# Kernel optimization log

Hardware: AMD Instinct MI355X
Metric: run time of the kernel (lower is better)

The kernel has to match this reference:

```python
import jax, jax.numpy as jnp
import numpy as np

BN_EPS = 1e-5


def _gin_layer(x, agg, W1, b1, W2, b2, gamma, beta):
    # GINConv with eps=0: h = MLP(x + sum_{j in N(i)} x_j)
    h = x + agg
    h = jax.nn.relu(h @ W1 + b1)
    h = jax.nn.relu(h @ W2 + b2)
    # BatchNorm1d, training mode (batch statistics, biased variance)
    mean = jnp.mean(h, axis=0)
    var = jnp.var(h, axis=0)
    return (h - mean) * jax.lax.rsqrt(var + BN_EPS) * gamma + beta


def setup_inputs() -> dict:
    key = jax.random.key(0)
    ks = jax.random.split(key, 10)
    N, E, D_IN, D_H, D_OUT = 100000, 1600000, 128, 128, 128
    s = lambda fi, fo: (2.0 / (fi + fo)) ** 0.5
    return {
        "x": jax.random.normal(ks[0], (N, D_IN), dtype=jnp.float32),
        "edge_index": jax.random.randint(ks[1], (2, E), 0, N, dtype=jnp.int64),
        "W1a": jax.random.normal(ks[2], (D_IN, D_H), dtype=jnp.float32) * s(D_IN, D_H),
        "b1a": jnp.zeros((D_H,), jnp.float32),
        "W1b": jax.random.normal(ks[3], (D_H, D_H), dtype=jnp.float32) * s(D_H, D_H),
        "b1b": jnp.zeros((D_H,), jnp.float32),
        "g1": jnp.ones((D_H,), jnp.float32),
        "be1": jnp.zeros((D_H,), jnp.float32),
        "W2a": jax.random.normal(ks[4], (D_H, D_H), dtype=jnp.float32) * s(D_H, D_H),
        "b2a": jnp.zeros((D_H,), jnp.float32),
        "W2b": jax.random.normal(ks[5], (D_H, D_OUT), dtype=jnp.float32) * s(D_H, D_OUT),
        "b2b": jnp.zeros((D_OUT,), jnp.float32),
        "g2": jnp.ones((D_OUT,), jnp.float32),
        "be2": jnp.zeros((D_OUT,), jnp.float32),
    }


def reference(x, edge_index, W1a, b1a, W1b, b1b, g1, be1,
              W2a, b2a, W2b, b2b, g2, be2):
    N = x.shape[0]
    src, dst = edge_index[0], edge_index[1]
    # layer 1: scatter-add neighbor features into targets
    agg = jax.ops.segment_sum(x[src], dst, num_segments=N)
    h = _gin_layer(x, agg, W1a, b1a, W1b, b1b, g1, be1)
    # layer 2
    agg = jax.ops.segment_sum(h[src], dst, num_segments=N)
    h = _gin_layer(h, agg, W2a, b2a, W2b, b2b, g2, be2)
    return h
```

## Files before the change

### kernel.cpp

```cpp
#include <hip/hip_runtime.h>
#include <hip/hip_bf16.h>

typedef unsigned int u32;
typedef unsigned short u16;
typedef short bf16x8 __attribute__((ext_vector_type(8)));
typedef float f32x4 __attribute__((ext_vector_type(4)));

static __device__ __forceinline__ float bf_lo(u32 v) { return __uint_as_float(v << 16); }
static __device__ __forceinline__ float bf_hi(u32 v) { return __uint_as_float(v & 0xffff0000u); }
static __device__ __forceinline__ u16 f2bf(float f) {
    u32 u = __float_as_uint(f);
    u32 r = u + 0x7fffu + ((u >> 16) & 1u);
    return (u16)(r >> 16);
}
static __device__ __forceinline__ u32 pack2(float a, float b) {
    return ((u32)f2bf(b) << 16) | (u32)f2bf(a);
}

__global__ __launch_bounds__(256) void convert_k(const float* __restrict__ in,
                                                 u32* __restrict__ out2, int total4)
{
    for (int i = blockIdx.x * 256 + threadIdx.x; i < total4; i += gridDim.x * 256) {
        float4 v = reinterpret_cast<const float4*>(in)[i];
        out2[2 * i + 0] = pack2(v.x, v.y);
        out2[2 * i + 1] = pack2(v.z, v.w);
    }
}

__global__ __launch_bounds__(256) void wprep_k(const float* __restrict__ Wa,
                                               const float* __restrict__ Wb,
                                               const float* __restrict__ Wc,
                                               const float* __restrict__ Wd,
                                               u16* __restrict__ Wf)
{
    int g = blockIdx.x * 256 + threadIdx.x;
    int which = g >> 14;
    int t = g & 16383;
    const float* W = which == 0 ? Wa : which == 1 ? Wb : which == 2 ? Wc : Wd;
    int j  = t & 7;
    int l  = (t >> 3) & 63;
    int nb = (t >> 9) & 7;
    int kg = (t >> 12) & 3;
    int k  = kg * 32 + (l >> 4) * 8 + j;
    int n  = nb * 16 + (l & 15);
    Wf[g] = f2bf(W[k * 128 + n]);
}

__global__ __launch_bounds__(256) void bhist_k(const int* __restrict__ edst,
                                               int* __restrict__ gcount, int E, int NB)
{
    __shared__ int lh[1024];
    for (int i = threadIdx.x; i < 1024; i += 256) lh[i] = 0;
    __syncthreads();
    for (int e = blockIdx.x * 256 + threadIdx.x; e < E; e += gridDim.x * 256)
        atomicAdd(&lh[edst[e] >> 7], 1);
    __syncthreads();
    for (int b = threadIdx.x; b < NB; b += 256)
        if (lh[b]) atomicAdd(&gcount[b], lh[b]);
}

__global__ __launch_bounds__(1024) void bscan_k(const int* __restrict__ gcount,
                                                int* __restrict__ goffs,
                                                int* __restrict__ gcur, int NB)
{
    __shared__ int s[1024];
    int t = threadIdx.x;
    int v = (t < NB) ? gcount[t] : 0;
    s[t] = v; __syncthreads();
    for (int d = 1; d < 1024; d <<= 1) {
        int x = (t >= d) ? s[t - d] : 0;
        __syncthreads();
        s[t] += x;
        __syncthreads();
    }
    if (t < NB) { int o = s[t] - v; goffs[t] = o; gcur[t] = o; }
    if (t == NB - 1) goffs[NB] = s[t];
}

__global__ __launch_bounds__(256) void bfill_k(const int* __restrict__ esrc,
                                               const int* __restrict__ edst,
                                               int* __restrict__ gcur,
                                               u32* __restrict__ bpacked, int E, int NB)
{
    __shared__ int lh[1024];
    __shared__ int lbase[1024];
    int t = threadIdx.x;
    for (int i = t; i < 1024; i += 256) lh[i] = 0;
    __syncthreads();
    int per = (E + gridDim.x - 1) / gridDim.x;
    int lo = blockIdx.x * per;
    int hi = lo + per; if (hi > E) hi = E;
    for (int e = lo + t; e < hi; e += 256) atomicAdd(&lh[edst[e] >> 7], 1);
    __syncthreads();
    for (int b = t; b < NB; b += 256) {
        int c = lh[b];
        lbase[b] = c ? atomicAdd(&gcur[b], c) : 0;
    }
    __syncthreads();
    for (int i = t; i < 1024; i += 256) lh[i] = 0;
    __syncthreads();
    for (int e = lo + t; e < hi; e += 256) {
        int d = edst[e];
        int b = d >> 7;
        int idx = atomicAdd(&lh[b], 1);
        bpacked[lbase[b] + idx] = ((u32)(d & 127) << 17) | (u32)esrc[e];
    }
}

__global__ __launch_bounds__(256) void fsort_k(const u32* __restrict__ bpacked,
                                               const int* __restrict__ goffs,
                                               int* __restrict__ slots,
                                               int* __restrict__ offs,
                                               int* __restrict__ deg, int N)
{
    __shared__ int cnt[128];
    __shared__ int roff[128];
    int b = blockIdx.x, t = threadIdx.x;
    int start = goffs[b], end = goffs[b + 1];
    if (t < 128) cnt[t] = 0;
    __syncthreads();
    for (int e = start + t; e < end; e += 256)
        atomicAdd(&cnt[bpacked[e] >> 17], 1);
    __syncthreads();
    if (t == 0) {
        int acc = 0;
        for (int i = 0; i < 128; ++i) { roff[i] = acc; acc += cnt[i]; }
    }
    __syncthreads();
    int row0 = b * 128;
    if (t < 128 && row0 + t < N) {
        offs[row0 + t] = start + roff[t];
        deg[row0 + t]  = cnt[t];
    }
    if (t < 128) cnt[t] = 0;
    __syncthreads();
    for (int e = start + t; e < end; e += 256) {
        u32 pk = bpacked[e];
        int local = (int)(pk >> 17);
        int idx = atomicAdd(&cnt[local], 1);
        slots[start + roff[local] + idx] = (int)(pk & 0x1FFFF);
    }
}

template<int MODE>
__global__ __launch_bounds__(256) void gather_k(const u32* __restrict__ xb2,
                                                const int* __restrict__ offs,
                                                const int* __restrict__ deg,
                                                const int* __restrict__ slots,
                                                const float* __restrict__ stats_in,
                                                const float* __restrict__ g_in,
                                                const float* __restrict__ be_in,
                                                u32* __restrict__ xa2, int N)
{
    __shared__ float sc[128], sh[128];
    int t = threadIdx.x;
    if (MODE == 1) {
        if (t < 128) {
            float invN = 1.0f / (float)N;
            float mean = stats_in[t] * invN;
            float var  = stats_in[128 + t] * invN - mean * mean;
            float s = g_in[t] * rsqrtf(var + 1e-5f);
            sc[t] = s;
            sh[t] = be_in[t] - mean * s;
        }
        __syncthreads();
    }

    int row = blockIdx.x * 4 + (t >> 6);
    if (row >= N) return;
    int lane = t & 63;

    u32 self = xb2[(size_t)row * 64 + lane];
    float ax0 = bf_lo(self), ay0 = bf_hi(self);
    float ax1 = 0.f, ay1 = 0.f;

    int start = offs[row];
    int dg = deg[row];
    for (int base = 0; base < dg; base += 64) {
        int rem = dg - base;
        int m = rem < 64 ? rem : 64;
        int slot = (lane < m) ? slots[start + base + lane] : 0;
        int j = 0;
        for (; j + 8 <= m; j += 8) {
            int s0 = __shfl(slot, j + 0);
            int s1 = __shfl(slot, j + 1);
            int s2 = __shfl(slot, j + 2);
            int s3 = __shfl(slot, j + 3);
            int s4 = __shfl(slot, j + 4);
            int s5 = __shfl(slot, j + 5);
            int s6 = __shfl(slot, j + 6);
            int s7 = __shfl(slot, j + 7);
            u32 v0 = xb2[(size_t)s0 * 64 + lane];
            u32 v1 = xb2[(size_t)s1 * 64 + lane];
            u32 v2 = xb2[(size_t)s2 * 64 + lane];
            u32 v3 = xb2[(size_t)s3 * 64 + lane];
            u32 v4 = xb2[(size_t)s4 * 64 + lane];
            u32 v5 = xb2[(size_t)s5 * 64 + lane];
            u32 v6 = xb2[(size_t)s6 * 64 + lane];
            u32 v7 = xb2[(size_t)s7 * 64 + lane];
            ax0 += bf_lo(v0); ay0 += bf_hi(v0);
            ax1 += bf_lo(v1); ay1 += bf_hi(v1);
            ax0 += bf_lo(v2); ay0 += bf_hi(v2);
            ax1 += bf_lo(v3); ay1 += bf_hi(v3);
            ax0 += bf_lo(v4); ay0 += bf_hi(v4);
            ax1 += bf_lo(v5); ay1 += bf_hi(v5);
            ax0 += bf_lo(v6); ay0 += bf_hi(v6);
            ax1 += bf_lo(v7); ay1 += bf_hi(v7);
        }
        for (; j < m; ++j) {
            int s = __shfl(slot, j);
            u32 v = xb2[(size_t)s * 64 + lane];
            ax0 += bf_lo(v);
            ay0 += bf_hi(v);
        }
    }
    float ax = ax0 + ax1, ay = ay0 + ay1;
    if (MODE == 1) {
        float d1 = (float)(dg + 1);
        ax = sc[2 * lane]     * ax + d1 * sh[2 * lane];
        ay = sc[2 * lane + 1] * ay + d1 * sh[2 * lane + 1];
    }
    xa2[(size_t)row * 64 + lane] = pack2(ax, ay);
}

template<int MODE>
__global__ __launch_bounds__(256) void mlp_mfma_k(
    const u16* __restrict__ xa,
    const u16* __restrict__ wfa, const float* __restrict__ ba,
    const u16* __restrict__ wfb, const float* __restrict__ bb,
    u16* __restrict__ hb_out, float* __restrict__ hf_out,
    float* __restrict__ partial, int N)
{
    __shared__ short ta[64 * 128];
    __shared__ float ssum[256];

    int t = threadIdx.x;
    int w = t >> 6, l = t & 63;
    int row0 = blockIdx.x * 64;

    for (int c = t; c < 1024; c += 256) {
        int r = c >> 4, ci = c & 15;
        int dst = (r * 128 + ci * 8) ^ ((r & 7) << 3);
        f32x4 v;
        if (row0 + r < N)
            v = *reinterpret_cast<const f32x4*>(xa + ((size_t)(row0 + r) * 128 + ci * 8));
        else
            v = f32x4{0.f, 0.f, 0.f, 0.f};
        *reinterpret_cast<f32x4*>(ta + dst) = v;
    }

    bf16x8 wf[2][4];
#pragma unroll
    for (int nr = 0; nr < 2; ++nr) {
        int nb = 2 * w + nr;
#pragma unroll
        for (int kg = 0; kg < 4; ++kg)
            wf[nr][kg] = *reinterpret_cast<const bf16x8*>(
                wfa + ((size_t)((kg * 8 + nb) * 64 + l)) * 8);
    }
    __syncthreads();

    int rr = l & 15;
    int kg8 = l >> 4;

    f32x4 acc[4][2];
#pragma unroll
    for (int mr = 0; mr < 4; ++mr)
#pragma unroll
        for (int nr = 0; nr < 2; ++nr)
            acc[mr][nr] = f32x4{0.f, 0.f, 0.f, 0.f};

#pragma unroll
    for (int mr = 0; mr < 4; ++mr) {
        int r = mr * 16 + rr;
        bf16x8 af[4];
#pragma unroll
        for (int kg = 0; kg < 4; ++kg) {
            int idx = (r * 128 + kg * 32 + kg8 * 8) ^ ((r & 7) << 3);
            af[kg] = *reinterpret_cast<const bf16x8*>(ta + idx);
        }
#pragma unroll
        for (int nr = 0; nr < 2; ++nr)
#pragma unroll
            for (int kg = 0; kg < 4; ++kg)
                acc[mr][nr] = __builtin_amdgcn_mfma_f32_16x16x32_bf16(
                    af[kg], wf[nr][kg], acc[mr][nr], 0, 0, 0);
    }
    __syncthreads();

    int colb = w * 32;
    float b0 = ba[colb + rr];
    float b1 = ba[colb + 16 + rr];
#pragma unroll
    for (int mr = 0; mr < 4; ++mr)
#pragma unroll
        for (int nr = 0; nr < 2; ++nr) {
            float bb_ = nr ? b1 : b0;
            int col = colb + nr * 16 + rr;
#pragma unroll
            for (int reg = 0; reg < 4; ++reg) {
                int row = mr * 16 + kg8 * 4 + reg;
                float v = fmaxf(acc[mr][nr][reg] + bb_, 0.0f);
                ta[(row * 128 + col) ^ ((row & 7) << 3)] = (short)f2bf(v);
            }
        }

#pragma unroll
    for (int nr = 0; nr < 2; ++nr) {
        int nb = 2 * w + nr;
#pragma unroll
        for (int kg = 0; kg < 4; ++kg)
            wf[nr][kg] = *reinterpret_cast<const bf16x8*>(
                wfb + ((size_t)((kg * 8 + nb) * 64 + l)) * 8);
    }
    __syncthreads();

#pragma unroll
    for (int mr = 0; mr < 4; ++mr)
#pragma unroll
        for (int nr = 0; nr < 2; ++nr)
            acc[mr][nr] = f32x4{0.f, 0.f, 0.f, 0.f};

#pragma unroll
    for (int mr = 0; mr < 4; ++mr) {
        int r = mr * 16 + rr;
        bf16x8 af[4];
#pragma unroll
        for (int kg = 0; kg < 4; ++kg) {
            int idx = (r * 128 + kg * 32 + kg8 * 8) ^ ((r & 7) << 3);
            af[kg] = *reinterpret_cast<const bf16x8*>(ta + idx);
        }
#pragma unroll
        for (int nr = 0; nr < 2; ++nr)
#pragma unroll
            for (int kg = 0; kg < 4; ++kg)
                acc[mr][nr] = __builtin_amdgcn_mfma_f32_16x16x32_bf16(
                    af[kg], wf[nr][kg], acc[mr][nr], 0, 0, 0);
    }

    float c0 = bb[colb + rr];
    float c1 = bb[colb + 16 + rr];
    float s0 = 0.f, q0 = 0.f, s1 = 0.f, q1 = 0.f;
#pragma unroll
    for (int mr = 0; mr < 4; ++mr) {
#pragma unroll
        for (int reg = 0; reg < 4; ++reg) {
            int row = row0 + mr * 16 + kg8 * 4 + reg;
            bool ok = row < N;
            float v0 = fmaxf(acc[mr][0][reg] + c0, 0.0f);
            float v1 = fmaxf(acc[mr][1][reg] + c1, 0.0f);
            if (ok) {
                if (MODE == 0) {
                    hb_out[(size_t)row * 128 + colb + rr]      = f2bf(v0);
                    hb_out[(size_t)row * 128 + colb + 16 + rr] = f2bf(v1);
                } else {
                    hf_out[(size_t)row * 128 + colb + rr]      = v0;
                    hf_out[(size_t)row * 128 + colb + 16 + rr] = v1;
                }
                s0 += v0; q0 += v0 * v0;
                s1 += v1; q1 += v1 * v1;
            }
        }
    }
    s0 += __shfl_xor(s0, 16); s0 += __shfl_xor(s0, 32);
    q0 += __shfl_xor(q0, 16); q0 += __shfl_xor(q0, 32);
    s1 += __shfl_xor(s1, 16); s1 += __shfl_xor(s1, 32);
    q1 += __shfl_xor(q1, 16); q1 += __shfl_xor(q1, 32);
    if (kg8 == 0) {
        ssum[colb + rr]            = s0;
        ssum[128 + colb + rr]      = q0;
        ssum[colb + 16 + rr]       = s1;
        ssum[128 + colb + 16 + rr] = q1;
    }
    __syncthreads();
    partial[(size_t)blockIdx.x * 256 + t] = ssum[t];
}

__global__ __launch_bounds__(256) void reduce_k(const float* __restrict__ partial,
                                                float* __restrict__ stats, int nrows)
{
    int t = threadIdx.x;
    int chunk = (nrows + gridDim.x - 1) / gridDim.x;
    int lo = blockIdx.x * chunk;
    int hi = lo + chunk; if (hi > nrows) hi = nrows;
    float acc = 0.f;
    for (int r = lo; r < hi; ++r)
        acc += partial[(size_t)r * 256 + t];
    if (hi > lo) atomicAdd(&stats[t], acc);
}

__global__ __launch_bounds__(256) void bn_apply_k(
    float* __restrict__ h, const float* __restrict__ stats,
    const float* __restrict__ gamma, const float* __restrict__ beta, int N)
{
    __shared__ float sc[128], sh[128];
    int t = threadIdx.x;
    if (t < 128) {
        float invN = 1.0f / (float)N;
        float mean = stats[t] * invN;
        float var  = stats[128 + t] * invN - mean * mean;
        float s = gamma[t] * rsqrtf(var + 1e-5f);
        sc[t] = s;
        sh[t] = beta[t] - mean * s;
    }
    __syncthreads();
    int total = N * 32;
    for (int i = blockIdx.x * 256 + t; i < total; i += gridDim.x * 256) {
        float4 v = reinterpret_cast<float4*>(h)[i];
        int c = (i & 31) * 4;
        v.x = v.x * sc[c + 0] + sh[c + 0];
        v.y = v.y * sc[c + 1] + sh[c + 1];
        v.z = v.z * sc[c + 2] + sh[c + 2];
        v.w = v.w * sc[c + 3] + sh[c + 3];
        reinterpret_cast<float4*>(h)[i] = v;
    }
}

extern "C" void kernel_launch(void* const* d_in, const int* in_sizes, int n_in,
                              void* d_out, int out_size, void* d_ws, size_t ws_size,
                              hipStream_t stream)
{
    const float* x   = (const float*)d_in[0];
    const int*   ei  = (const int*)d_in[1];
    const float* W1a = (const float*)d_in[2];
    const float* b1a = (const float*)d_in[3];
    const float* W1b = (const float*)d_in[4];
    const float* b1b = (const float*)d_in[5];
    const float* g1  = (const float*)d_in[6];
    const float* be1 = (const float*)d_in[7];
    const float* W2a = (const float*)d_in[8];
    const float* b2a = (const float*)d_in[9];
    const float* W2b = (const float*)d_in[10];
    const float* b2b = (const float*)d_in[11];
    const float* g2  = (const float*)d_in[12];
    const float* be2 = (const float*)d_in[13];

    const int N = in_sizes[0] / 128;
    const int E = in_sizes[1] / 2;
    const int* esrc = ei;
    const int* edst = ei + E;
    const int NB = (N + 127) >> 7;

    const int mblocks = (N + 63) / 64;
    const int gblocks = (N + 3) / 4;

    char* p = (char*)d_ws;
    const size_t featb = (size_t)N * 128 * sizeof(u16);
    u16* xa = (u16*)p;            p += featb;
    u16* h1 = (u16*)p;            p += featb;
    u16* xb = (u16*)p;            p += featb;
    u16* wf = (u16*)p;            p += 4 * 16384 * sizeof(u16);
    int* slots = (int*)p;         p += (size_t)E * sizeof(int);
    int* deg   = (int*)p;         p += (size_t)N * sizeof(int);
    int* offs  = (int*)p;         p += (size_t)N * sizeof(int);
    int* gcount = (int*)p;        p += 1024 * sizeof(int);
    int* goffs  = (int*)p;        p += 1032 * sizeof(int);
    int* gcur   = (int*)p;        p += 1024 * sizeof(int);
    float* stats = (float*)p;     p += 512 * sizeof(float);
    float* partial = (float*)p;   p += (size_t)mblocks * 256 * sizeof(float);
    u32* bpacked = (u32*)xa;

    u16* wf1a = wf;
    u16* wf1b = wf + 16384;
    u16* wf2a = wf + 32768;
    u16* wf2b = wf + 49152;
    float* stats1 = stats;
    float* stats2 = stats + 256;

    float* h = (float*)d_out;

    hipMemsetAsync(gcount, 0, 1024 * sizeof(int), stream);
    bhist_k<<<256, 256, 0, stream>>>(edst, gcount, E, NB);
    bscan_k<<<1, 1024, 0, stream>>>(gcount, goffs, gcur, NB);
    bfill_k<<<256, 256, 0, stream>>>(esrc, edst, gcur, bpacked, E, NB);
    fsort_k<<<NB, 256, 0, stream>>>(bpacked, goffs, slots, offs, deg, N);
    convert_k<<<2048, 256, 0, stream>>>(x, (u32*)xb, N * 32);
    wprep_k<<<256, 256, 0, stream>>>(W1a, W1b, W2a, W2b, wf);
    hipMemsetAsync(stats, 0, 512 * sizeof(float), stream);

    gather_k<0><<<gblocks, 256, 0, stream>>>((const u32*)xb, offs, deg, slots,
                                             nullptr, nullptr, nullptr, (u32*)xa, N);
    mlp_mfma_k<0><<<mblocks, 256, 0, stream>>>(xa, wf1a, b1a, wf1b, b1b,
                                               h1, (float*)nullptr, partial, N);
    reduce_k<<<32, 256, 0, stream>>>(partial, stats1, mblocks);

    gather_k<1><<<gblocks, 256, 0, stream>>>((const u32*)h1, offs, deg, slots,
                                             stats1, g1, be1, (u32*)xa, N);
    mlp_mfma_k<1><<<mblocks, 256, 0, stream>>>(xa, wf2a, b2a, wf2b, b2b,
                                               (u16*)nullptr, h, partial, N);
    reduce_k<<<32, 256, 0, stream>>>(partial, stats2, mblocks);

    bn_apply_k<<<2048, 256, 0, stream>>>(h, stats2, g2, be2, N);
}
```

Before: 299.2 us.

## Use scalar slot loads in gather, bf16 layer-2 output, parallel scan in fsort

The gather kernel now makes the row's offset and degree wave-uniform and loads neighbor indices as scalar loads instead of shuffling them. It unrolls the neighbor loop 16 wide with four accumulator pairs and uses byte-shift addressing for rows. The second MLP now writes bf16 into the h1 buffer instead of fp32 to the output, and a new BN-apply kernel reads bf16 and writes fp32, cutting the intermediate write traffic. fsort's serial per-block prefix sum becomes a parallel Hillis-Steele scan. Storing the pre-BN layer-2 activations in bf16 adds rounding error to the final output.

```diff
diff --git a/kernel.cpp b/kernel.cpp
--- a/kernel.cpp
+++ b/kernel.cpp
@@ -115,6 +115,7 @@
 {
     __shared__ int cnt[128];
     __shared__ int roff[128];
+    __shared__ int sb[128];
     int b = blockIdx.x, t = threadIdx.x;
     int start = goffs[b], end = goffs[b + 1];
     if (t < 128) cnt[t] = 0;
@@ -122,10 +123,15 @@
     for (int e = start + t; e < end; e += 256)
         atomicAdd(&cnt[bpacked[e] >> 17], 1);
     __syncthreads();
-    if (t == 0) {
-        int acc = 0;
-        for (int i = 0; i < 128; ++i) { roff[i] = acc; acc += cnt[i]; }
-    }
+    if (t < 128) sb[t] = cnt[t];
+    __syncthreads();
+    for (int d = 1; d < 128; d <<= 1) {
+        int x = (t < 128 && t >= d) ? sb[t - d] : 0;
+        __syncthreads();
+        if (t < 128) sb[t] += x;
+        __syncthreads();
+    }
+    if (t < 128) roff[t] = sb[t] - cnt[t];
     __syncthreads();
     int row0 = b * 128;
     if (t < 128 && row0 + t < N) {
@@ -141,6 +147,8 @@
         slots[start + roff[local] + idx] = (int)(pk & 0x1FFFF);
     }
 }
+
+#define ROWP(s) reinterpret_cast<const u32*>(xbase + ((size_t)(u32)(s) << 8))
 
 template<int MODE>
 __global__ __launch_bounds__(256) void gather_k(const u32* __restrict__ xb2,
@@ -169,67 +177,87 @@
     int row = blockIdx.x * 4 + (t >> 6);
     if (row >= N) return;
     int lane = t & 63;
-
-    u32 self = xb2[(size_t)row * 64 + lane];
+    const char* xbase = (const char*)xb2;
+
+    u32 self = ROWP(row)[lane];
     float ax0 = bf_lo(self), ay0 = bf_hi(self);
-    float ax1 = 0.f, ay1 = 0.f;
-
-    int start = offs[row];
-    int dg = deg[row];
-    for (int base = 0; base < dg; base += 64) {
-        int rem = dg - base;
-        int m = rem < 64 ? rem : 64;
-        int slot = (lane < m) ? slots[start + base + lane] : 0;
-        int j = 0;
-        for (; j + 8 <= m; j += 8) {
-            int s0 = __shfl(slot, j + 0);
-            int s1 = __shfl(slot, j + 1);
-            int s2 = __shfl(slot, j + 2);
-            int s3 = __shfl(slot, j + 3);
-            int s4 = __shfl(slot, j + 4);
-            int s5 = __shfl(slot, j + 5);
-            int s6 = __shfl(slot, j + 6);
-            int s7 = __shfl(slot, j + 7);
-            u32 v0 = xb2[(size_t)s0 * 64 + lane];
-            u32 v1 = xb2[(size_t)s1 * 64 + lane];
-            u32 v2 = xb2[(size_t)s2 * 64 + lane];
-            u32 v3 = xb2[(size_t)s3 * 64 + lane];
-            u32 v4 = xb2[(size_t)s4 * 64 + lane];
-            u32 v5 = xb2[(size_t)s5 * 64 + lane];
-            u32 v6 = xb2[(size_t)s6 * 64 + lane];
-            u32 v7 = xb2[(size_t)s7 * 64 + lane];
-            ax0 += bf_lo(v0); ay0 += bf_hi(v0);
-            ax1 += bf_lo(v1); ay1 += bf_hi(v1);
-            ax0 += bf_lo(v2); ay0 += bf_hi(v2);
-            ax1 += bf_lo(v3); ay1 += bf_hi(v3);
-            ax0 += bf_lo(v4); ay0 += bf_hi(v4);
-            ax1 += bf_lo(v5); ay1 += bf_hi(v5);
-            ax0 += bf_lo(v6); ay0 += bf_hi(v6);
-            ax1 += bf_lo(v7); ay1 += bf_hi(v7);
-        }
-        for (; j < m; ++j) {
-            int s = __shfl(slot, j);
-            u32 v = xb2[(size_t)s * 64 + lane];
-            ax0 += bf_lo(v);
-            ay0 += bf_hi(v);
-        }
-    }
-    float ax = ax0 + ax1, ay = ay0 + ay1;
+    float ax1 = 0.f, ay1 = 0.f, ax2 = 0.f, ay2 = 0.f, ax3 = 0.f, ay3 = 0.f;
+
+    int ustart = __builtin_amdgcn_readfirstlane(offs[row]);
+    int udg    = __builtin_amdgcn_readfirstlane(deg[row]);
+
+    int e = 0;
+    for (; e + 16 <= udg; e += 16) {
+        int s0 = slots[ustart + e + 0],  s1 = slots[ustart + e + 1];
+        int s2 = slots[ustart + e + 2],  s3 = slots[ustart + e + 3];
+        int s4 = slots[ustart + e + 4],  s5 = slots[ustart + e + 5];
+        int s6 = slots[ustart + e + 6],  s7 = slots[ustart + e + 7];
+        int s8 = slots[ustart + e + 8],  s9 = slots[ustart + e + 9];
+        int sA = slots[ustart + e + 10], sB = slots[ustart + e + 11];
+        int sC = slots[ustart + e + 12], sD = slots[ustart + e + 13];
+        int sE = slots[ustart + e + 14], sF = slots[ustart + e + 15];
+        u32 v0 = ROWP(s0)[lane], v1 = ROWP(s1)[lane];
+        u32 v2 = ROWP(s2)[lane], v3 = ROWP(s3)[lane];
+        u32 v4 = ROWP(s4)[lane], v5 = ROWP(s5)[lane];
+        u32 v6 = ROWP(s6)[lane], v7 = ROWP(s7)[lane];
+        u32 v8 = ROWP(s8)[lane], v9 = ROWP(s9)[lane];
+        u32 vA = ROWP(sA)[lane], vB = ROWP(sB)[lane];
+        u32 vC = ROWP(sC)[lane], vD = ROWP(sD)[lane];
+        u32 vE = ROWP(sE)[lane], vF = ROWP(sF)[lane];
+        ax0 += bf_lo(v0); ay0 += bf_hi(v0);  ax1 += bf_lo(v1); ay1 += bf_hi(v1);
+        ax2 += bf_lo(v2); ay2 += bf_hi(v2);  ax3 += bf_lo(v3); ay3 += bf_hi(v3);
+        ax0 += bf_lo(v4); ay0 += bf_hi(v4);  ax1 += bf_lo(v5); ay1 += bf_hi(v5);
+        ax2 += bf_lo(v6); ay2 += bf_hi(v6);  ax3 += bf_lo(v7); ay3 += bf_hi(v7);
+        ax0 += bf_lo(v8); ay0 += bf_hi(v8);  ax1 += bf_lo(v9); ay1 += bf_hi(v9);
+        ax2 += bf_lo(vA); ay2 += bf_hi(vA);  ax3 += bf_lo(vB); ay3 += bf_hi(vB);
+        ax0 += bf_lo(vC); ay0 += bf_hi(vC);  ax1 += bf_lo(vD); ay1 += bf_hi(vD);
+        ax2 += bf_lo(vE); ay2 += bf_hi(vE);  ax3 += bf_lo(vF); ay3 += bf_hi(vF);
+    }
+    if (e + 8 <= udg) {
+        int s0 = slots[ustart + e + 0], s1 = slots[ustart + e + 1];
+        int s2 = slots[ustart + e + 2], s3 = slots[ustart + e + 3];
+        int s4 = slots[ustart + e + 4], s5 = slots[ustart + e + 5];
+        int s6 = slots[ustart + e + 6], s7 = slots[ustart + e + 7];
+        u32 v0 = ROWP(s0)[lane], v1 = ROWP(s1)[lane];
+        u32 v2 = ROWP(s2)[lane], v3 = ROWP(s3)[lane];
+        u32 v4 = ROWP(s4)[lane], v5 = ROWP(s5)[lane];
+        u32 v6 = ROWP(s6)[lane], v7 = ROWP(s7)[lane];
+        ax0 += bf_lo(v0); ay0 += bf_hi(v0);  ax1 += bf_lo(v1); ay1 += bf_hi(v1);
+        ax2 += bf_lo(v2); ay2 += bf_hi(v2);  ax3 += bf_lo(v3); ay3 += bf_hi(v3);
+        ax0 += bf_lo(v4); ay0 += bf_hi(v4);  ax1 += bf_lo(v5); ay1 += bf_hi(v5);
+        ax2 += bf_lo(v6); ay2 += bf_hi(v6);  ax3 += bf_lo(v7); ay3 += bf_hi(v7);
+        e += 8;
+    }
+    if (e + 4 <= udg) {
+        int s0 = slots[ustart + e + 0], s1 = slots[ustart + e + 1];
+        int s2 = slots[ustart + e + 2], s3 = slots[ustart + e + 3];
+        u32 v0 = ROWP(s0)[lane], v1 = ROWP(s1)[lane];
+        u32 v2 = ROWP(s2)[lane], v3 = ROWP(s3)[lane];
+        ax0 += bf_lo(v0); ay0 += bf_hi(v0);  ax1 += bf_lo(v1); ay1 += bf_hi(v1);
+        ax2 += bf_lo(v2); ay2 += bf_hi(v2);  ax3 += bf_lo(v3); ay3 += bf_hi(v3);
+        e += 4;
+    }
+    for (; e < udg; ++e) {
+        int s = slots[ustart + e];
+        u32 v = ROWP(s)[lane];
+        ax0 += bf_lo(v); ay0 += bf_hi(v);
+    }
+
+    float ax = (ax0 + ax1) + (ax2 + ax3);
+    float ay = (ay0 + ay1) + (ay2 + ay3);
     if (MODE == 1) {
-        float d1 = (float)(dg + 1);
+        float d1 = (float)(udg + 1);
         ax = sc[2 * lane]     * ax + d1 * sh[2 * lane];
         ay = sc[2 * lane + 1] * ay + d1 * sh[2 * lane + 1];
     }
     xa2[(size_t)row * 64 + lane] = pack2(ax, ay);
 }
 
-template<int MODE>
 __global__ __launch_bounds__(256) void mlp_mfma_k(
     const u16* __restrict__ xa,
     const u16* __restrict__ wfa, const float* __restrict__ ba,
     const u16* __restrict__ wfb, const float* __restrict__ bb,
-    u16* __restrict__ hb_out, float* __restrict__ hf_out,
-    float* __restrict__ partial, int N)
+    u16* __restrict__ hb_out, float* __restrict__ partial, int N)
 {
     __shared__ short ta[64 * 128];
     __shared__ float ssum[256];
@@ -350,13 +378,8 @@
             float v0 = fmaxf(acc[mr][0][reg] + c0, 0.0f);
             float v1 = fmaxf(acc[mr][1][reg] + c1, 0.0f);
             if (ok) {
-                if (MODE == 0) {
-                    hb_out[(size_t)row * 128 + colb + rr]      = f2bf(v0);
-                    hb_out[(size_t)row * 128 + colb + 16 + rr] = f2bf(v1);
-                } else {
-                    hf_out[(size_t)row * 128 + colb + rr]      = v0;
-                    hf_out[(size_t)row * 128 + colb + 16 + rr] = v1;
-                }
+                hb_out[(size_t)row * 128 + colb + rr]      = f2bf(v0);
+                hb_out[(size_t)row * 128 + colb + 16 + rr] = f2bf(v1);
                 s0 += v0; q0 += v0 * v0;
                 s1 += v1; q1 += v1 * v1;
             }
@@ -389,9 +412,10 @@
     if (hi > lo) atomicAdd(&stats[t], acc);
 }
 
-__global__ __launch_bounds__(256) void bn_apply_k(
-    float* __restrict__ h, const float* __restrict__ stats,
-    const float* __restrict__ gamma, const float* __restrict__ beta, int N)
+__global__ __launch_bounds__(256) void bn_apply_bf_k(
+    const u32* __restrict__ h2b, const float* __restrict__ stats,
+    const float* __restrict__ gamma, const float* __restrict__ beta,
+    float* __restrict__ out, int N)
 {
     __shared__ float sc[128], sh[128];
     int t = threadIdx.x;
@@ -404,15 +428,14 @@
         sh[t] = beta[t] - mean * s;
     }
     __syncthreads();
-    int total = N * 32;
-    for (int i = blockIdx.x * 256 + t; i < total; i += gridDim.x * 256) {
-        float4 v = reinterpret_cast<float4*>(h)[i];
-        int c = (i & 31) * 4;
-        v.x = v.x * sc[c + 0] + sh[c + 0];
-        v.y = v.y * sc[c + 1] + sh[c + 1];
-        v.z = v.z * sc[c + 2] + sh[c + 2];
-        v.w = v.w * sc[c + 3] + sh[c + 3];
-        reinterpret_cast<float4*>(h)[i] = v;
+    int total2 = N * 64;
+    for (int i = blockIdx.x * 256 + t; i < total2; i += gridDim.x * 256) {
+        u32 v = h2b[i];
+        int c = (i & 63) * 2;
+        float2 o;
+        o.x = bf_lo(v) * sc[c]     + sh[c];
+        o.y = bf_hi(v) * sc[c + 1] + sh[c + 1];
+        reinterpret_cast<float2*>(out)[i] = o;
     }
 }
 
@@ -450,7 +473,7 @@
     u16* h1 = (u16*)p;            p += featb;
     u16* xb = (u16*)p;            p += featb;
     u16* wf = (u16*)p;            p += 4 * 16384 * sizeof(u16);
-    int* slots = (int*)p;         p += (size_t)E * sizeof(int);
+    int* slots = (int*)p;         p += (size_t)E * sizeof(int) + 64;
     int* deg   = (int*)p;         p += (size_t)N * sizeof(int);
     int* offs  = (int*)p;         p += (size_t)N * sizeof(int);
     int* gcount = (int*)p;        p += 1024 * sizeof(int);
@@ -480,15 +503,15 @@
 
     gather_k<0><<<gblocks, 256, 0, stream>>>((const u32*)xb, offs, deg, slots,
                                              nullptr, nullptr, nullptr, (u32*)xa, N);
-    mlp_mfma_k<0><<<mblocks, 256, 0, stream>>>(xa, wf1a, b1a, wf1b, b1b,
-                                               h1, (float*)nullptr, partial, N);
+    mlp_mfma_k<<<mblocks, 256, 0, stream>>>(xa, wf1a, b1a, wf1b, b1b,
+                                            h1, partial, N);
     reduce_k<<<32, 256, 0, stream>>>(partial, stats1, mblocks);
 
     gather_k<1><<<gblocks, 256, 0, stream>>>((const u32*)h1, offs, deg, slots,
                                              stats1, g1, be1, (u32*)xa, N);
-    mlp_mfma_k<1><<<mblocks, 256, 0, stream>>>(xa, wf2a, b2a, wf2b, b2b,
-                                               (u16*)nullptr, h, partial, N);
+    mlp_mfma_k<<<mblocks, 256, 0, stream>>>(xa, wf2a, b2a, wf2b, b2b,
+                                            h1, partial, N);
     reduce_k<<<32, 256, 0, stream>>>(partial, stats2, mblocks);
 
-    bn_apply_k<<<2048, 256, 0, stream>>>(h, stats2, g2, be2, N);
-}
+    bn_apply_bf_k<<<2048, 256, 0, stream>>>((const u32*)h1, stats2, g2, be2, h, N);
+}
```

Result: faster. 281.9 us (-5.8%).
